# Performance work log

Hardware: AMD Instinct MI355X
Metric: run time of the kernel (lower is better)

The kernel has to match this reference:

```python
import jax, jax.numpy as jnp
import numpy as np

B, S, DM, H = 4, 2048, 512, 8
HD = DM // H


def setup_inputs() -> dict:
    key = jax.random.key(0)
    ks = jax.random.split(key, 12)
    x = jax.random.normal(ks[0], (B, S, DM), dtype=jnp.float32)
    # causal lower-triangular mask [B, S, S]
    mask = jnp.broadcast_to(jnp.tril(jnp.ones((S, S), dtype=jnp.int32)), (B, S, S))
    # sorted irregular day offsets (trading-day-like), in days
    days_offset = jnp.sort(
        jax.random.uniform(ks[1], (B, S), dtype=jnp.float32) * 3000.0, axis=-1
    )
    scale = 1.0 / np.sqrt(DM)
    Wq = jax.random.normal(ks[2], (DM, DM), dtype=jnp.float32) * scale
    bq = jnp.zeros((DM,), dtype=jnp.float32)
    Wk = jax.random.normal(ks[3], (DM, DM), dtype=jnp.float32) * scale
    bk = jnp.zeros((DM,), dtype=jnp.float32)
    Wv = jax.random.normal(ks[4], (DM, DM), dtype=jnp.float32) * scale
    bv = jnp.zeros((DM,), dtype=jnp.float32)
    Wo = jax.random.normal(ks[5], (DM, DM), dtype=jnp.float32) * scale
    bo = jnp.zeros((DM,), dtype=jnp.float32)
    decay_rate = jnp.float32(0.1)
    return {
        "x": x, "mask": mask, "days_offset": days_offset,
        "Wq": Wq, "bq": bq, "Wk": Wk, "bk": bk,
        "Wv": Wv, "bv": bv, "Wo": Wo, "bo": bo,
        "decay_rate": decay_rate,
    }


def reference(x, mask, days_offset, Wq, bq, Wk, bk, Wv, bv, Wo, bo, decay_rate):
    b, s, _ = x.shape
    # projections (torch Linear: x @ W.T + b), split heads -> [b, h, s, hd]
    def proj(W, bias):
        return (x @ W.T + bias).reshape(b, s, H, HD).transpose(0, 2, 1, 3)
    q, k, v = proj(Wq, bq), proj(Wk, bk), proj(Wv, bv)
    scores = jnp.einsum("bhqd,bhkd->bhqk", q, k) / jnp.sqrt(jnp.float32(HD))
    # temporal decay: exp(-rate * |t_i - t_j|), broadcast over heads
    dist = jnp.abs(days_offset[:, :, None] - days_offset[:, None, :])  # [b,s,s]
    decay = jnp.exp(-decay_rate * dist)
    scores = scores * decay[:, None, :, :]
    scores = jnp.where(mask[:, None, :, :] == 0, -jnp.inf, scores)
    attn = jax.nn.softmax(scores, axis=-1)  # dropout p=0 (eval)
    out = jnp.einsum("bhqk,bhkd->bhqd", attn, v)
    out = out.transpose(0, 2, 1, 3).reshape(b, s, DM)
    return out @ Wo.T + bo
```

## Files before the change

### kernel.cpp

```cpp
#include <hip/hip_runtime.h>
#include <hip/hip_fp16.h>


#define S_LEN 2048
#define DMODEL 512
#define NH 8
#define HD 64

typedef _Float16 half8 __attribute__((ext_vector_type(8)));
typedef _Float16 half4 __attribute__((ext_vector_type(4)));
typedef float floatx4 __attribute__((ext_vector_type(4)));

__device__ __forceinline__ void gload16(const _Float16* g, _Float16* l) {
    __builtin_amdgcn_global_load_lds(
        (const __attribute__((address_space(1))) void*)g,
        (__attribute__((address_space(3))) void*)l, 16, 0, 0);
}

__device__ __forceinline__ half8 cvt8(float4 a, float4 b) {
    half8 h;
    h[0] = (_Float16)a.x; h[1] = (_Float16)a.y; h[2] = (_Float16)a.z; h[3] = (_Float16)a.w;
    h[4] = (_Float16)b.x; h[5] = (_Float16)b.y; h[6] = (_Float16)b.z; h[7] = (_Float16)b.w;
    return h;
}

__device__ __forceinline__ void stage_f32(
    const float* __restrict__ src, _Float16* __restrict__ dstbase,
    int row, int sw, int lane7, int kcol)
{
    const float* p = src + (size_t)row * DMODEL + kcol + sw * 8;
    float4 a = *(const float4*)p;
    float4 b = *(const float4*)(p + 4);
    *(half8*)(dstbase + row * 64 + lane7 * 8) = cvt8(a, b);
}

__global__ __launch_bounds__(256) void qkv_gemm(
    const float* __restrict__ x,
    const float* __restrict__ Wq, const float* __restrict__ Wk, const float* __restrict__ Wv,
    const float* __restrict__ bq, const float* __restrict__ bk, const float* __restrict__ bv,
    _Float16* __restrict__ outh)
{
    __shared__ _Float16 As[2][128 * 64];
    __shared__ _Float16 Ws[2][128 * 64];
    const int t = threadIdx.x;
    const int bm = blockIdx.x, bn = blockIdx.y, z = blockIdx.z;
    const float* Wp = (z == 0) ? Wq : (z == 1) ? Wk : Wv;
    const float* bias = (z == 0) ? bq : (z == 1) ? bk : bv;
    const int w = t >> 6, lane = t & 63, l15 = lane & 15, quad = lane >> 4;
    const int wrow = (w >> 1) * 64, wcol = (w & 1) * 64;
    const int lrow = lane >> 3, lane7 = lane & 7;
    const int sw = lane7 ^ lrow;
    const float* xb = x  + (size_t)(bm * 128) * DMODEL;
    const float* Wb = Wp + (size_t)(bn * 128) * DMODEL;

    auto stage = [&](int kb, int buf) {
        #pragma unroll
        for (int i = 0; i < 4; ++i) {
            int row = w * 32 + i * 8 + lrow;
            stage_f32(xb, As[buf], row, sw, lane7, kb * 64);
            stage_f32(Wb, Ws[buf], row, sw, lane7, kb * 64);
        }
    };

    floatx4 acc[4][4] = {};
    stage(0, 0);
    for (int kb = 0; kb < 8; ++kb) {
        const int buf = kb & 1;
        __syncthreads();
        if (kb < 7) stage(kb + 1, buf ^ 1);
        #pragma unroll
        for (int kk = 0; kk < 2; ++kk) {
            half8 xf[4], wf[4];
            #pragma unroll
            for (int mt = 0; mt < 4; ++mt)
                xf[mt] = *(const half8*)(&As[buf][(wrow + mt * 16 + l15) * 64 + (((quad + 4 * kk) ^ (l15 & 7)) * 8)]);
            #pragma unroll
            for (int nt = 0; nt < 4; ++nt)
                wf[nt] = *(const half8*)(&Ws[buf][(wcol + nt * 16 + l15) * 64 + (((quad + 4 * kk) ^ (l15 & 7)) * 8)]);
            if (z == 2) {
                #pragma unroll
                for (int mt = 0; mt < 4; ++mt)
                    #pragma unroll
                    for (int nt = 0; nt < 4; ++nt)
                        acc[mt][nt] = __builtin_amdgcn_mfma_f32_16x16x32_f16(xf[mt], wf[nt], acc[mt][nt], 0, 0, 0);
            } else {
                #pragma unroll
                for (int nt = 0; nt < 4; ++nt)
                    #pragma unroll
                    for (int mt = 0; mt < 4; ++mt)
                        acc[nt][mt] = __builtin_amdgcn_mfma_f32_16x16x32_f16(wf[nt], xf[mt], acc[nt][mt], 0, 0, 0);
            }
        }
    }

    if (z == 2) {
        #pragma unroll
        for (int mt = 0; mt < 4; ++mt)
            #pragma unroll
            for (int nt = 0; nt < 4; ++nt) {
                int n = bn * 128 + wcol + nt * 16 + l15;
                float bvv = bias[n];
                int m0 = bm * 128 + wrow + mt * 16 + quad * 4;
                int b = m0 >> 11, s0 = m0 & 2047;
                int hh = n >> 6, hd = n & 63;
                half4 hv;
                #pragma unroll
                for (int r = 0; r < 4; ++r) hv[r] = (_Float16)(acc[mt][nt][r] + bvv);
                *(half4*)(outh + (size_t)2 * (8192 * 512) +
                          ((size_t)(b * NH + hh) * HD + hd) * S_LEN + s0) = hv;
            }
    } else {
        #pragma unroll
        for (int nt = 0; nt < 4; ++nt)
            #pragma unroll
            for (int mt = 0; mt < 4; ++mt) {
                int n0 = bn * 128 + wcol + nt * 16 + quad * 4;
                float4 b4 = *(const float4*)(bias + n0);
                int m = bm * 128 + wrow + mt * 16 + l15;
                int b = m >> 11, s = m & 2047;
                int hh = n0 >> 6, hd0 = n0 & 63;
                half4 hv;
                hv[0] = (_Float16)(acc[nt][mt][0] + b4.x);
                hv[1] = (_Float16)(acc[nt][mt][1] + b4.y);
                hv[2] = (_Float16)(acc[nt][mt][2] + b4.z);
                hv[3] = (_Float16)(acc[nt][mt][3] + b4.w);
                *(half4*)(outh + (size_t)z * (8192 * 512) +
                          ((size_t)(b * NH + hh) * S_LEN + s) * HD + hd0) = hv;
            }
    }
}

__global__ __launch_bounds__(256) void out_gemm(
    const _Float16* __restrict__ A, const float* __restrict__ Wo,
    const float* __restrict__ bo, float* __restrict__ outf)
{
    __shared__ _Float16 As[2][64 * 64];
    __shared__ _Float16 Ws[2][128 * 64];
    const int t = threadIdx.x;
    const int bm = blockIdx.x, bn = blockIdx.y;
    const int w = t >> 6, lane = t & 63, l15 = lane & 15, quad = lane >> 4;
    const int wn = w * 32;
    const int lrow = lane >> 3, lane7 = lane & 7;
    const int sw = lane7 ^ lrow;
    const _Float16* Ab = A  + (size_t)(bm * 64) * DMODEL;
    const float*    Wb = Wo + (size_t)(bn * 128) * DMODEL;

    auto stage = [&](int kb, int buf) {
        #pragma unroll
        for (int i = 0; i < 2; ++i) {
            int row = (w * 2 + i) * 8 + lrow;
            gload16(Ab + (size_t)row * DMODEL + kb * 64 + sw * 8, &As[buf][row * 64]);
        }
        #pragma unroll
        for (int i = 0; i < 4; ++i)
            stage_f32(Wb, Ws[buf], w * 32 + i * 8 + lrow, sw, lane7, kb * 64);
    };

    floatx4 acc[2][4] = {};
    stage(0, 0);
    for (int kb = 0; kb < 8; ++kb) {
        const int buf = kb & 1;
        __syncthreads();
        if (kb < 7) stage(kb + 1, buf ^ 1);
        #pragma unroll
        for (int kk = 0; kk < 2; ++kk) {
            half8 wf[2], af[4];
            #pragma unroll
            for (int nt = 0; nt < 2; ++nt)
                wf[nt] = *(const half8*)(&Ws[buf][(wn + nt * 16 + l15) * 64 + (((quad + 4 * kk) ^ (l15 & 7)) * 8)]);
            #pragma unroll
            for (int mt = 0; mt < 4; ++mt)
                af[mt] = *(const half8*)(&As[buf][(mt * 16 + l15) * 64 + (((quad + 4 * kk) ^ (l15 & 7)) * 8)]);
            #pragma unroll
            for (int nt = 0; nt < 2; ++nt)
                #pragma unroll
                for (int mt = 0; mt < 4; ++mt)
                    acc[nt][mt] = __builtin_amdgcn_mfma_f32_16x16x32_f16(wf[nt], af[mt], acc[nt][mt], 0, 0, 0);
        }
    }

    #pragma unroll
    for (int nt = 0; nt < 2; ++nt)
        #pragma unroll
        for (int mt = 0; mt < 4; ++mt) {
            int n0 = bn * 128 + wn + nt * 16 + quad * 4;
            float4 b4 = *(const float4*)(bo + n0);
            int m = bm * 64 + mt * 16 + l15;
            float4 v;
            v.x = acc[nt][mt][0] + b4.x; v.y = acc[nt][mt][1] + b4.y;
            v.z = acc[nt][mt][2] + b4.z; v.w = acc[nt][mt][3] + b4.w;
            *(float4*)(outf + (size_t)m * DMODEL + n0) = v;
        }
}

__global__ __launch_bounds__(256, 2) void attn_k(
    const _Float16* __restrict__ Qh, const _Float16* __restrict__ Kh,
    const _Float16* __restrict__ Vt, const float* __restrict__ days,
    const float* __restrict__ rate_p, _Float16* __restrict__ Ah)
{
    __shared__ _Float16 Ks[2][64 * 64];
    __shared__ _Float16 Vs[2][64 * 64];
    __shared__ float    eks[2][64];
    __shared__ _Float16 Ps[4][16 * 64];

    const int h = blockIdx.x, pr = blockIdx.y, b = blockIdx.z;
    const int t = threadIdx.x, w = t >> 6, lane = t & 63, l15 = lane & 15, quad = lane >> 4;
    const float rate = rate_p[0];
    const size_t bhoff = (size_t)(b * NH + h) * (size_t)(S_LEN * HD);
    const _Float16* Qb = Qh + bhoff;
    const _Float16* Kb = Kh + bhoff;
    const _Float16* Vb = Vt + bhoff;
    const float* daysb = days + b * S_LEN;
    const int lrow = lane >> 3, sw = (lane & 7) ^ lrow;
    const int e7 = l15 & 7;

    auto stage = [&](int kt, int buf) {
        #pragma unroll
        for (int i = 0; i < 2; ++i) {
            int grp = w * 2 + i;
            int row = grp * 8 + lrow;
            gload16(Kb + (size_t)(kt * 64 + row) * HD + sw * 8, &Ks[buf][grp * 512]);
            gload16(Vb + (size_t)row * S_LEN + kt * 64 + sw * 8, &Vs[buf][grp * 512]);
        }
        if (w == 0) {
            float tk0 = daysb[kt * 64];
            float d = daysb[kt * 64 + lane];
            eks[buf][lane] = __expf(fminf(rate * (d - tk0), 80.f));
        }
    };

    auto run_phase = [&](int j, int par0, int nextj) -> int {
        const int qg = j * 64 + w * 16 + l15;
        half8 qf0 = *(const half8*)(Qb + (size_t)qg * HD + quad * 8);
        half8 qf1 = *(const half8*)(Qb + (size_t)qg * HD + 32 + quad * 8);
        const float tq = daysb[qg];
        floatx4 oacc[4] = {};
        float lacc = 0.f;

        for (int kt = 0; kt <= j; ++kt) {
            const int par = (par0 + kt) & 1;
            __syncthreads();
            if (kt < j) stage(kt + 1, par ^ 1);
            else if (nextj >= 0) stage(0, par ^ 1);
            const float tk0 = daysb[kt * 64];
            half8 kf[4][2];
            #pragma unroll
            for (int c = 0; c < 4; ++c)
                #pragma unroll
                for (int kk = 0; kk < 2; ++kk)
                    kf[c][kk] = *(const half8*)(&Ks[par][(c * 16 + l15) * 64 + (((quad + 4 * kk) ^ e7) * 8)]);
            floatx4 sc[4];
            #pragma unroll
            for (int c = 0; c < 4; ++c) {
                floatx4 z4 = {};
                z4 = __builtin_amdgcn_mfma_f32_16x16x32_f16(kf[c][0], qf0, z4, 0, 0, 0);
                sc[c] = __builtin_amdgcn_mfma_f32_16x16x32_f16(kf[c][1], qf1, z4, 0, 0, 0);
            }
            half8 vf[4][2];
            #pragma unroll
            for (int s4 = 0; s4 < 4; ++s4)
                #pragma unroll
                for (int kk = 0; kk < 2; ++kk)
                    vf[s4][kk] = *(const half8*)(&Vs[par][(s4 * 16 + l15) * 64 + (((quad + 4 * kk) ^ e7) * 8)]);
            const float eq = 0.125f * __expf(-rate * (tq - tk0));
            floatx4 eqk[4];
            #pragma unroll
            for (int c = 0; c < 4; ++c)
                eqk[c] = eq * *(const floatx4*)(&eks[par][c * 16 + quad * 4]);
            if (kt == j) {
                #pragma unroll
                for (int c = 0; c < 4; ++c) {
                    float pvv[4];
                    #pragma unroll
                    for (int r = 0; r < 4; ++r) {
                        float p = __expf(sc[c][r] * eqk[c][r]);
                        if ((kt * 64 + c * 16 + quad * 4 + r) > qg) p = 0.f;
                        lacc += p;
                        pvv[r] = p;
                    }
                    half4 hv;
                    hv[0] = (_Float16)pvv[0]; hv[1] = (_Float16)pvv[1];
                    hv[2] = (_Float16)pvv[2]; hv[3] = (_Float16)pvv[3];
                    *(half4*)(&Ps[w][l15 * 64 + (((2 * c + (quad >> 1)) ^ e7) * 8) + (quad & 1) * 4]) = hv;
                }
            } else {
                #pragma unroll
                for (int c = 0; c < 4; ++c) {
                    float pvv[4];
                    #pragma unroll
                    for (int r = 0; r < 4; ++r) {
                        float p = __expf(sc[c][r] * eqk[c][r]);
                        lacc += p;
                        pvv[r] = p;
                    }
                    half4 hv;
                    hv[0] = (_Float16)pvv[0]; hv[1] = (_Float16)pvv[1];
                    hv[2] = (_Float16)pvv[2]; hv[3] = (_Float16)pvv[3];
                    *(half4*)(&Ps[w][l15 * 64 + (((2 * c + (quad >> 1)) ^ e7) * 8) + (quad & 1) * 4]) = hv;
                }
            }
            half8 pf0 = *(const half8*)(&Ps[w][l15 * 64 + ((quad ^ e7) * 8)]);
            half8 pf1 = *(const half8*)(&Ps[w][l15 * 64 + (((4 + quad) ^ e7) * 8)]);
            #pragma unroll
            for (int s4 = 0; s4 < 4; ++s4) {
                oacc[s4] = __builtin_amdgcn_mfma_f32_16x16x32_f16(vf[s4][0], pf0, oacc[s4], 0, 0, 0);
                oacc[s4] = __builtin_amdgcn_mfma_f32_16x16x32_f16(vf[s4][1], pf1, oacc[s4], 0, 0, 0);
            }
        }

        float l = lacc;
        l += __shfl_xor(l, 16);
        l += __shfl_xor(l, 32);
        float linv = 1.0f / l;
        #pragma unroll
        for (int s4 = 0; s4 < 4; ++s4) {
            half4 hv;
            #pragma unroll
            for (int r = 0; r < 4; ++r) hv[r] = (_Float16)(oacc[s4][r] * linv);
            *(half4*)(Ah + ((size_t)(b * S_LEN) + qg) * DMODEL + h * HD + s4 * 16 + quad * 4) = hv;
        }
        return (par0 + j + 1) & 1;
    };

    const int j0 = pr, j1 = 31 - pr;
    stage(0, 0);
    int p1 = run_phase(j0, 0, j1);
    run_phase(j1, p1, -1);
}

extern "C" void kernel_launch(void* const* d_in, const int* in_sizes, int n_in,
                              void* d_out, int out_size, void* d_ws, size_t ws_size,
                              hipStream_t stream)
{
    const float* x    = (const float*)d_in[0];
    const float* days = (const float*)d_in[2];
    const float* Wq   = (const float*)d_in[3];
    const float* bq   = (const float*)d_in[4];
    const float* Wk   = (const float*)d_in[5];
    const float* bk   = (const float*)d_in[6];
    const float* Wv   = (const float*)d_in[7];
    const float* bv   = (const float*)d_in[8];
    const float* Wo   = (const float*)d_in[9];
    const float* bo   = (const float*)d_in[10];
    const float* rate = (const float*)d_in[11];
    float* out = (float*)d_out;

    _Float16* Qh = (_Float16*)d_ws;
    _Float16* Kh = Qh + 4194304;
    _Float16* Vh = Kh + 4194304;
    _Float16* Ah = Vh + 4194304;

    dim3 g0(64, 4, 3);
    qkv_gemm<<<g0, 256, 0, stream>>>(x, Wq, Wk, Wv, bq, bk, bv, Qh);

    dim3 ga(NH, 16, 4);
    attn_k<<<ga, 256, 0, stream>>>(Qh, Kh, Vh, days, rate, Ah);

    dim3 g1(128, 4, 1);
    out_gemm<<<g1, 256, 0, stream>>>(Ah, Wo, bo, out);
}
```

Baseline: 207.3 us.

## Software-pipeline QK^T of next key tile with softmax and PV of current tile

```diff
diff --git a/kernel.cpp b/kernel.cpp
--- a/kernel.cpp
+++ b/kernel.cpp
@@ -237,67 +237,51 @@
         floatx4 oacc[4] = {};
         float lacc = 0.f;
 
-        for (int kt = 0; kt <= j; ++kt) {
-            const int par = (par0 + kt) & 1;
-            __syncthreads();
-            if (kt < j) stage(kt + 1, par ^ 1);
-            else if (nextj >= 0) stage(0, par ^ 1);
-            const float tk0 = daysb[kt * 64];
+        floatx4 scA[4], scB[4], eqA[4], eqB[4];
+        half8 vfA[4][2], vfB[4][2];
+
+        auto load_tile = [&](int kt, int par, floatx4 (&sc)[4],
+                             half8 (&vf)[4][2], floatx4 (&eqk)[4]) {
             half8 kf[4][2];
             #pragma unroll
             for (int c = 0; c < 4; ++c)
                 #pragma unroll
                 for (int kk = 0; kk < 2; ++kk)
                     kf[c][kk] = *(const half8*)(&Ks[par][(c * 16 + l15) * 64 + (((quad + 4 * kk) ^ e7) * 8)]);
-            floatx4 sc[4];
             #pragma unroll
             for (int c = 0; c < 4; ++c) {
                 floatx4 z4 = {};
                 z4 = __builtin_amdgcn_mfma_f32_16x16x32_f16(kf[c][0], qf0, z4, 0, 0, 0);
                 sc[c] = __builtin_amdgcn_mfma_f32_16x16x32_f16(kf[c][1], qf1, z4, 0, 0, 0);
             }
-            half8 vf[4][2];
             #pragma unroll
             for (int s4 = 0; s4 < 4; ++s4)
                 #pragma unroll
                 for (int kk = 0; kk < 2; ++kk)
                     vf[s4][kk] = *(const half8*)(&Vs[par][(s4 * 16 + l15) * 64 + (((quad + 4 * kk) ^ e7) * 8)]);
+            const float tk0 = daysb[kt * 64];
             const float eq = 0.125f * __expf(-rate * (tq - tk0));
-            floatx4 eqk[4];
             #pragma unroll
             for (int c = 0; c < 4; ++c)
                 eqk[c] = eq * *(const floatx4*)(&eks[par][c * 16 + quad * 4]);
-            if (kt == j) {
-                #pragma unroll
-                for (int c = 0; c < 4; ++c) {
-                    float pvv[4];
-                    #pragma unroll
-                    for (int r = 0; r < 4; ++r) {
-                        float p = __expf(sc[c][r] * eqk[c][r]);
-                        if ((kt * 64 + c * 16 + quad * 4 + r) > qg) p = 0.f;
-                        lacc += p;
-                        pvv[r] = p;
-                    }
-                    half4 hv;
-                    hv[0] = (_Float16)pvv[0]; hv[1] = (_Float16)pvv[1];
-                    hv[2] = (_Float16)pvv[2]; hv[3] = (_Float16)pvv[3];
-                    *(half4*)(&Ps[w][l15 * 64 + (((2 * c + (quad >> 1)) ^ e7) * 8) + (quad & 1) * 4]) = hv;
+        };
+
+        auto softmax_pv = [&](floatx4 (&sc)[4], half8 (&vf)[4][2],
+                              floatx4 (&eqk)[4], bool dg, int kt) {
+            #pragma unroll
+            for (int c = 0; c < 4; ++c) {
+                float pvv[4];
+                #pragma unroll
+                for (int r = 0; r < 4; ++r) {
+                    float p = __expf(sc[c][r] * eqk[c][r]);
+                    if (dg && (kt * 64 + c * 16 + quad * 4 + r) > qg) p = 0.f;
+                    lacc += p;
+                    pvv[r] = p;
                 }
-            } else {
-                #pragma unroll
-                for (int c = 0; c < 4; ++c) {
-                    float pvv[4];
-                    #pragma unroll
-                    for (int r = 0; r < 4; ++r) {
-                        float p = __expf(sc[c][r] * eqk[c][r]);
-                        lacc += p;
-                        pvv[r] = p;
-                    }
-                    half4 hv;
-                    hv[0] = (_Float16)pvv[0]; hv[1] = (_Float16)pvv[1];
-                    hv[2] = (_Float16)pvv[2]; hv[3] = (_Float16)pvv[3];
-                    *(half4*)(&Ps[w][l15 * 64 + (((2 * c + (quad >> 1)) ^ e7) * 8) + (quad & 1) * 4]) = hv;
-                }
+                half4 hv;
+                hv[0] = (_Float16)pvv[0]; hv[1] = (_Float16)pvv[1];
+                hv[2] = (_Float16)pvv[2]; hv[3] = (_Float16)pvv[3];
+                *(half4*)(&Ps[w][l15 * 64 + (((2 * c + (quad >> 1)) ^ e7) * 8) + (quad & 1) * 4]) = hv;
             }
             half8 pf0 = *(const half8*)(&Ps[w][l15 * 64 + ((quad ^ e7) * 8)]);
             half8 pf1 = *(const half8*)(&Ps[w][l15 * 64 + (((4 + quad) ^ e7) * 8)]);
@@ -306,6 +290,39 @@
                 oacc[s4] = __builtin_amdgcn_mfma_f32_16x16x32_f16(vf[s4][0], pf0, oacc[s4], 0, 0, 0);
                 oacc[s4] = __builtin_amdgcn_mfma_f32_16x16x32_f16(vf[s4][1], pf1, oacc[s4], 0, 0, 0);
             }
+        };
+
+        auto stage_next = [&](int kt, int par) {
+            if (kt < j) stage(kt + 1, par ^ 1);
+            else if (nextj >= 0) stage(0, par ^ 1);
+        };
+
+        __syncthreads();
+        stage_next(0, par0);
+        load_tile(0, par0, scA, vfA, eqA);
+
+        int kt = 1;
+        for (; kt + 1 <= j; kt += 2) {
+            int p1 = (par0 + kt) & 1;
+            __syncthreads();
+            stage_next(kt, p1);
+            load_tile(kt, p1, scB, vfB, eqB);
+            softmax_pv(scA, vfA, eqA, false, kt - 1);
+            int p2 = p1 ^ 1;
+            __syncthreads();
+            stage_next(kt + 1, p2);
+            load_tile(kt + 1, p2, scA, vfA, eqA);
+            softmax_pv(scB, vfB, eqB, false, kt);
+        }
+        if (kt <= j) {
+            int p1 = (par0 + kt) & 1;
+            __syncthreads();
+            stage_next(kt, p1);
+            load_tile(kt, p1, scB, vfB, eqB);
+            softmax_pv(scA, vfA, eqA, false, kt - 1);
+            softmax_pv(scB, vfB, eqB, true, j);
+        } else {
+            softmax_pv(scA, vfA, eqA, true, j);
         }
 
         float l = lacc;
```

After: 205.2 us. No clear change (-1.0%).
